# Performance work log

Hardware: AMD Instinct MI355X
Metric: run time of the kernel (lower is better)

## Reference

```python
import jax, jax.numpy as jnp
import numpy as np

B, T, I, H, L, HPR = 256, 512, 128, 256, 64, 50


def _mlp(x, W1, b1, W2, b2):
    # Linear -> ReLU -> Linear, torch convention y = x @ W.T + b
    return jax.nn.relu(x @ W1.T + b1) @ W2.T + b2


def setup_inputs() -> dict:
    key = jax.random.key(0)
    ks = jax.random.split(key, 16)
    s = 0.05
    return {
        "x": jax.random.uniform(ks[0], (B, T, I), dtype=jnp.float32),
        "hidden": jnp.zeros((B, H), jnp.float32),
        "noise": jax.random.normal(ks[1], (B, T, L), dtype=jnp.float32),
        "Wpm1": s * jax.random.normal(ks[2], (HPR, H)), "bpm1": jnp.zeros((HPR,)),
        "Wpm2": s * jax.random.normal(ks[3], (L, HPR)), "bpm2": jnp.zeros((L,)),
        "Wpl1": s * jax.random.normal(ks[4], (HPR, H)), "bpl1": jnp.zeros((HPR,)),
        "Wpl2": s * jax.random.normal(ks[5], (L, HPR)), "bpl2": jnp.zeros((L,)),
        "Wqm1": s * jax.random.normal(ks[6], (HPR, I + H)), "bqm1": jnp.zeros((HPR,)),
        "Wqm2": s * jax.random.normal(ks[7], (L, HPR)), "bqm2": jnp.zeros((L,)),
        "Wql1": s * jax.random.normal(ks[8], (HPR, I + H)), "bql1": jnp.zeros((HPR,)),
        "Wql2": s * jax.random.normal(ks[9], (L, HPR)), "bql2": jnp.zeros((L,)),
        "Wh1": s * jax.random.normal(ks[10], (HPR, I + H + L)), "bh1": jnp.zeros((HPR,)),
        "Wh2": s * jax.random.normal(ks[11], (H, HPR)), "bh2": jnp.zeros((H,)),
        "Wo": s * jax.random.normal(ks[12], (I, H + L)), "bo": jnp.zeros((I,)),
    }


def reference(x, hidden, noise,
              Wpm1, bpm1, Wpm2, bpm2, Wpl1, bpl1, Wpl2, bpl2,
              Wqm1, bqm1, Wqm2, bqm2, Wql1, bql1, Wql2, bql2,
              Wh1, bh1, Wh2, bh2, Wo, bo):
    def step(h, inp):
        x_t, eps = inp  # [B,I], [B,L]
        xh = jnp.concatenate([x_t, h], axis=1)
        q_mu = _mlp(xh, Wqm1, bqm1, Wqm2, bqm2)
        q_lv = _mlp(xh, Wql1, bql1, Wql2, bql2)
        p_mu = _mlp(h, Wpm1, bpm1, Wpm2, bpm2)
        p_lv = _mlp(h, Wpl1, bpl1, Wpl2, bpl2)
        z = q_mu + jnp.exp(0.5 * q_lv) * eps
        h_next = _mlp(jnp.concatenate([x_t, h, z], axis=1), Wh1, bh1, Wh2, bh2)
        out = jax.nn.sigmoid(jnp.concatenate([h, z], axis=1) @ Wo.T + bo)
        return h_next, (out, p_mu, p_lv, q_mu, q_lv)

    xs = (jnp.swapaxes(x, 0, 1), jnp.swapaxes(noise, 0, 1))  # [T,B,*]
    _, (x_hat, p_mu, p_lv, q_mu, q_lv) = jax.lax.scan(step, hidden, xs)
    tb = lambda a: jnp.swapaxes(a, 0, 1)  # [T,B,*] -> [B,T,*]
    return tb(x_hat), tb(p_mu), tb(p_lv), tb(q_mu), tb(q_lv)
```

## Files before the change

### kernel.cpp

```cpp
#include <hip/hip_runtime.h>
#include <stdint.h>


typedef _Float16 f16x2 __attribute__((ext_vector_type(2)));

__device__ __forceinline__ float bf2f(uint16_t u) {
  union { uint32_t u; float f; } c; c.u = ((uint32_t)u) << 16; return c.f;
}
__device__ __forceinline__ uint16_t f2bf(float f) {
  union { float f; uint32_t u; } c; c.f = f;
  uint32_t u = c.u;
  uint32_t r = (u + 0x7FFFu + ((u >> 16) & 1u)) >> 16;
  return (uint16_t)r;
}
__device__ __forceinline__ uint32_t packh2(float a, float b) {
  union { f16x2 h; uint32_t u; } c;
  c.h.x = (_Float16)a; c.h.y = (_Float16)b; return c.u;
}
__device__ __forceinline__ float fdot2(uint32_t a, uint32_t b, float c) {
  union { uint32_t u; f16x2 h; } ua, ub; ua.u = a; ub.u = b;
#if __has_builtin(__builtin_amdgcn_fdot2)
  return __builtin_amdgcn_fdot2(ua.h, ub.h, c, false);
#else
  return c + (float)ua.h.x * (float)ub.h.x + (float)ua.h.y * (float)ub.h.y;
#endif
}

template <int CTRL>
__device__ __forceinline__ float dpp_mov(float x) {
#if __has_builtin(__builtin_amdgcn_update_dpp)
  union { float f; int i; } a, b;
  a.f = x;
  b.i = __builtin_amdgcn_update_dpp(0, a.i, CTRL, 0xF, 0xF, true);
  return b.f;
#else
  return __shfl_xor(x, (CTRL == 0xB1) ? 1 : (CTRL == 0x4E) ? 2 : 4);
#endif
}
__device__ __forceinline__ float red2(float x) {
  return x + dpp_mov<0xB1>(x);
}
__device__ __forceinline__ float red4(float x) {
  x += dpp_mov<0xB1>(x); x += dpp_mov<0x4E>(x); return x;
}
__device__ __forceinline__ float red8(float x) {
  x += dpp_mov<0xB1>(x); x += dpp_mov<0x4E>(x); x += dpp_mov<0x141>(x); return x;
}

__device__ __forceinline__ void barrier_lds() {
  asm volatile("s_waitcnt lgkmcnt(0)\n\ts_barrier" ::: "memory");
}

__device__ __forceinline__ int sniff_bf16(const uint32_t* xw) {
  int cnt = 0;
#pragma unroll
  for (int i = 0; i < 64; ++i) {
    uint32_t e = (xw[i] >> 7) & 0xFFu;
    cnt += (e >= 0x70u && e <= 0x7Fu) ? 1 : 0;
  }
  return cnt >= 32;
}
__device__ __forceinline__ float loadIn(const void* p, size_t i, int isbf) {
  return isbf ? bf2f(((const uint16_t*)p)[i]) : ((const float*)p)[i];
}
__device__ __forceinline__ void storeOut(void* p, size_t i, float v, int isbf) {
  if (isbf) ((uint16_t*)p)[i] = f2bf(v);
  else      ((float*)p)[i] = v;
}

#define WS_W2   75776
#define WS_BIAS 94208
#define N_JOBS  95168

struct PrepArgs {
  const void* W[11];
  const void* B[11];
  const uint32_t* xw;
};

__global__ void vrnn_prep(PrepArgs a, uint32_t* __restrict__ ws) {
  const int isbf = sniff_bf16(a.xw);
  int j = blockIdx.x * 256 + threadIdx.x;
  if (j < 75776) {
    int p = j >> 9, tid = j & 511;
    int t8 = tid >> 3, c8 = tid & 7;
    const void* W; int row, k, K; bool valid;
    if (p < 24)       { W = a.W[0]; row = t8; k = c8*48 + p*2;        K = 384; valid = row < 50; }
    else if (p < 48)  { W = a.W[1]; row = t8; k = c8*48 + (p-24)*2;   K = 384; valid = row < 50; }
    else if (p < 64)  { W = a.W[2]; row = t8; k = c8*32 + (p-48)*2;   K = 256; valid = row < 50; }
    else if (p < 80)  { W = a.W[3]; row = t8; k = c8*32 + (p-64)*2;   K = 256; valid = row < 50; }
    else if (p < 104) { W = a.W[4]; row = t8; k = c8*48 + (p-80)*2;   K = 448; valid = row < 50; }
    else if (p < 108) { W = a.W[4]; row = t8; k = 384 + c8*8 + (p-104)*2; K = 448; valid = row < 50; }
    else if (p < 124) { W = a.W[5]; row = t8;      k = c8*32 + (p-108)*2;     K = 320; valid = true; }
    else if (p < 128) { W = a.W[5]; row = t8;      k = 256 + c8*8 + (p-124)*2; K = 320; valid = true; }
    else if (p < 144) { W = a.W[5]; row = 64 + t8; k = c8*32 + (p-128)*2;     K = 320; valid = true; }
    else              { W = a.W[5]; row = 64 + t8; k = 256 + c8*8 + (p-144)*2; K = 320; valid = true; }
    float f0 = valid ? loadIn(W, (size_t)row * K + k, isbf)     : 0.f;
    float f1 = valid ? loadIn(W, (size_t)row * K + k + 1, isbf) : 0.f;
    ws[j] = packh2(f0, f1);
  } else if (j < WS_BIAS) {
    int q = j - WS_W2;
    const void* W; int r, kp;
    if (q < 9216) { int m = q / 2304, rem = q % 2304; r = rem / 36; kp = rem % 36; W = a.W[6 + m]; }
    else          { int rem = q - 9216;               r = rem / 36; kp = rem % 36; W = a.W[10]; }
    uint32_t v = 0;
    if (kp < 25) v = packh2(loadIn(W, r * 50 + kp * 2, isbf),
                            loadIn(W, r * 50 + kp * 2 + 1, isbf));
    ws[j] = v;
  } else if (j < N_JOBS) {
    int q = j - WS_BIAS; float v = 0.f;
    if (q < 320)      { int m = q >> 6, i = q & 63; if (i < 50) v = loadIn(a.B[m], i, isbf); }
    else if (q < 576) { int m = (q - 320) >> 6;     v = loadIn(a.B[5 + m], q & 63, isbf); }
    else if (q < 832) { v = loadIn(a.B[9],  q - 576, isbf); }
    else              { v = loadIn(a.B[10], q - 832, isbf); }
    ((float*)ws)[j] = v;
  }
}

__global__ __launch_bounds__(512, 2) void vrnn_main(
    const void* __restrict__ x, const void* __restrict__ hidden,
    const void* __restrict__ noise, const uint32_t* __restrict__ ws,
    void* __restrict__ out)
{
  __shared__ __align__(16) uint32_t s_w2[18432];
  __shared__ float s_bias[960];
  __shared__ __align__(16) _Float16 s_v[448];
  __shared__ __align__(16) uint32_t s_actu[180];
  _Float16* s_act = (_Float16*)s_actu;

  const int tid = threadIdx.x;
  const int b = blockIdx.x;
  const int isbf = sniff_bf16((const uint32_t*)x);

  uint32_t wqm1[24], wql1[24], wpm1[16], wpl1[16];
  uint32_t wh1a[24], wh1z[4], wo0h[16], wo0z[4], wo1h[16], wo1z[4];
#pragma unroll
  for (int i = 0; i < 24; ++i) wqm1[i] = ws[(0   + i) * 512 + tid];
#pragma unroll
  for (int i = 0; i < 24; ++i) wql1[i] = ws[(24  + i) * 512 + tid];
#pragma unroll
  for (int i = 0; i < 16; ++i) wpm1[i] = ws[(48  + i) * 512 + tid];
#pragma unroll
  for (int i = 0; i < 16; ++i) wpl1[i] = ws[(64  + i) * 512 + tid];
#pragma unroll
  for (int i = 0; i < 24; ++i) wh1a[i] = ws[(80  + i) * 512 + tid];
#pragma unroll
  for (int i = 0; i < 4;  ++i) wh1z[i] = ws[(104 + i) * 512 + tid];
#pragma unroll
  for (int i = 0; i < 16; ++i) wo0h[i] = ws[(108 + i) * 512 + tid];
#pragma unroll
  for (int i = 0; i < 4;  ++i) wo0z[i] = ws[(124 + i) * 512 + tid];
#pragma unroll
  for (int i = 0; i < 16; ++i) wo1h[i] = ws[(128 + i) * 512 + tid];
#pragma unroll
  for (int i = 0; i < 4;  ++i) wo1z[i] = ws[(144 + i) * 512 + tid];

  for (int i = tid; i < 18432; i += 512) s_w2[i] = ws[WS_W2 + i];
  {
    const float* wsf = (const float*)(ws + WS_BIAS);
    for (int i = tid; i < 960; i += 512) s_bias[i] = wsf[i];
  }

  if (tid < 128)      s_v[tid] = (_Float16)loadIn(x, (size_t)b * 65536 + tid, isbf);
  else if (tid < 384) s_v[tid] = (_Float16)loadIn(hidden, (size_t)b * 256 + (tid - 128), isbf);
  else if (tid < 448) s_v[tid] = (_Float16)0.f;

  const int row8 = tid >> 3, c8 = tid & 7;
  const int i2 = tid >> 2, c4 = tid & 3;
  const int rh = tid >> 1, ch = tid & 1;
  const uint4* v4 = (const uint4*)s_v;

  float eps_r = 0.f;
  if (c4 == 0 && i2 < 64) eps_r = loadIn(noise, (size_t)b * 32768 + i2, isbf);
  float xnext = 0.f;

  __syncthreads();

  const size_t OFF_PMU = 16777216u;
  const size_t OFF_PLV = 25165824u;
  const size_t OFF_QMU = 33554432u;
  const size_t OFF_QLV = 41943040u;

#pragma unroll 1
  for (int t = 0; t < 512; ++t) {
    const size_t bt = (size_t)b * 512 + t;
    if (tid >= 384) {
      int tn = (t < 511) ? t + 1 : 511;
      xnext = loadIn(x, ((size_t)b * 512 + tn) * 128 + (tid - 384), isbf);
    }

    float a_qm = 0.f, a_ql = 0.f, a_hx = 0.f;
    {
      const int g = c8 * 6;
#pragma unroll
      for (int i = 0; i < 6; ++i) {
        uint4 q = v4[g + i];
        a_qm = fdot2(wqm1[4*i+0], q.x, a_qm); a_ql = fdot2(wql1[4*i+0], q.x, a_ql); a_hx = fdot2(wh1a[4*i+0], q.x, a_hx);
        a_qm = fdot2(wqm1[4*i+1], q.y, a_qm); a_ql = fdot2(wql1[4*i+1], q.y, a_ql); a_hx = fdot2(wh1a[4*i+1], q.y, a_hx);
        a_qm = fdot2(wqm1[4*i+2], q.z, a_qm); a_ql = fdot2(wql1[4*i+2], q.z, a_ql); a_hx = fdot2(wh1a[4*i+2], q.z, a_hx);
        a_qm = fdot2(wqm1[4*i+3], q.w, a_qm); a_ql = fdot2(wql1[4*i+3], q.w, a_ql); a_hx = fdot2(wh1a[4*i+3], q.w, a_hx);
      }
    }
    float a_pm = 0.f, a_pl = 0.f, a_o0 = 0.f, a_o1 = 0.f;
    {
      const int g = 16 + c8 * 4;
#pragma unroll
      for (int i = 0; i < 4; ++i) {
        uint4 q = v4[g + i];
        a_pm = fdot2(wpm1[4*i+0], q.x, a_pm); a_pl = fdot2(wpl1[4*i+0], q.x, a_pl);
        a_o0 = fdot2(wo0h[4*i+0], q.x, a_o0); a_o1 = fdot2(wo1h[4*i+0], q.x, a_o1);
        a_pm = fdot2(wpm1[4*i+1], q.y, a_pm); a_pl = fdot2(wpl1[4*i+1], q.y, a_pl);
        a_o0 = fdot2(wo0h[4*i+1], q.y, a_o0); a_o1 = fdot2(wo1h[4*i+1], q.y, a_o1);
        a_pm = fdot2(wpm1[4*i+2], q.z, a_pm); a_pl = fdot2(wpl1[4*i+2], q.z, a_pl);
        a_o0 = fdot2(wo0h[4*i+2], q.z, a_o0); a_o1 = fdot2(wo1h[4*i+2], q.z, a_o1);
        a_pm = fdot2(wpm1[4*i+3], q.w, a_pm); a_pl = fdot2(wpl1[4*i+3], q.w, a_pl);
        a_o0 = fdot2(wo0h[4*i+3], q.w, a_o0); a_o1 = fdot2(wo1h[4*i+3], q.w, a_o1);
      }
    }
    a_qm = red8(a_qm); a_ql = red8(a_ql); a_pm = red8(a_pm); a_pl = red8(a_pl);
    if (c8 == 0) {
      s_act[row8]       = (_Float16)fmaxf(a_qm + s_bias[row8],       0.f);
      s_act[72 + row8]  = (_Float16)fmaxf(a_ql + s_bias[64 + row8],  0.f);
      s_act[144 + row8] = (_Float16)fmaxf(a_pm + s_bias[128 + row8], 0.f);
      s_act[216 + row8] = (_Float16)fmaxf(a_pl + s_bias[192 + row8], 0.f);
    }
    barrier_lds();

    {
      const bool isq = i2 < 64;
      const int r = isq ? i2 : i2 - 64;
      const uint32_t* Wm = s_w2 + (isq ? 0 : 4608) + r * 36 + c4 * 8;
      const uint32_t* Wl = s_w2 + (isq ? 2304 : 6912) + r * 36 + c4 * 8;
      const uint32_t* am = s_actu + (isq ? 0 : 72) + c4 * 8;
      const uint32_t* al = s_actu + (isq ? 36 : 108) + c4 * 8;
      uint4 wm0 = *(const uint4*)Wm, wm1 = *(const uint4*)(Wm + 4);
      uint4 wl0 = *(const uint4*)Wl, wl1 = *(const uint4*)(Wl + 4);
      uint4 am0 = *(const uint4*)am, am1 = *(const uint4*)(am + 4);
      uint4 al0 = *(const uint4*)al, al1 = *(const uint4*)(al + 4);
      float mu0 = 0.f, mu1 = 0.f, lv0 = 0.f, lv1 = 0.f;
      mu0 = fdot2(wm0.x, am0.x, mu0); lv0 = fdot2(wl0.x, al0.x, lv0);
      mu1 = fdot2(wm1.x, am1.x, mu1); lv1 = fdot2(wl1.x, al1.x, lv1);
      mu0 = fdot2(wm0.y, am0.y, mu0); lv0 = fdot2(wl0.y, al0.y, lv0);
      mu1 = fdot2(wm1.y, am1.y, mu1); lv1 = fdot2(wl1.y, al1.y, lv1);
      mu0 = fdot2(wm0.z, am0.z, mu0); lv0 = fdot2(wl0.z, al0.z, lv0);
      mu1 = fdot2(wm1.z, am1.z, mu1); lv1 = fdot2(wl1.z, al1.z, lv1);
      mu0 = fdot2(wm0.w, am0.w, mu0); lv0 = fdot2(wl0.w, al0.w, lv0);
      mu1 = fdot2(wm1.w, am1.w, mu1); lv1 = fdot2(wl1.w, al1.w, lv1);
      float mu = red4(mu0 + mu1);
      float lv = red4(lv0 + lv1);
      if (c4 == 0) {
        mu += s_bias[(isq ? 320 : 448) + r];
        lv += s_bias[(isq ? 384 : 512) + r];
        storeOut(out, (isq ? OFF_QMU : OFF_PMU) + bt * 64 + r, mu, isbf);
        storeOut(out, (isq ? OFF_QLV : OFF_PLV) + bt * 64 + r, lv, isbf);
        if (isq) {
          float z = mu + __expf(0.5f * lv) * eps_r;
          s_v[384 + r] = (_Float16)z;
          int tn = (t < 511) ? t + 1 : 511;
          eps_r = loadIn(noise, ((size_t)b * 512 + tn) * 64 + r, isbf);
        }
      }
    }
    barrier_lds();

    {
      uint4 qz = v4[48 + c8];
      float ah = a_hx, o0 = a_o0, o1 = a_o1;
      ah = fdot2(wh1z[0], qz.x, ah); o0 = fdot2(wo0z[0], qz.x, o0); o1 = fdot2(wo1z[0], qz.x, o1);
      ah = fdot2(wh1z[1], qz.y, ah); o0 = fdot2(wo0z[1], qz.y, o0); o1 = fdot2(wo1z[1], qz.y, o1);
      ah = fdot2(wh1z[2], qz.z, ah); o0 = fdot2(wo0z[2], qz.z, o0); o1 = fdot2(wo1z[2], qz.z, o1);
      ah = fdot2(wh1z[3], qz.w, ah); o0 = fdot2(wo0z[3], qz.w, o0); o1 = fdot2(wo1z[3], qz.w, o1);
      ah = red8(ah); o0 = red8(o0); o1 = red8(o1);
      if (c8 == 0) {
        s_act[288 + row8] = (_Float16)fmaxf(ah + s_bias[256 + row8], 0.f);
        float s0 = 1.f / (1.f + __expf(-(o0 + s_bias[832 + row8])));
        float s1 = 1.f / (1.f + __expf(-(o1 + s_bias[896 + row8])));
        storeOut(out, bt * 128 + row8, s0, isbf);
        storeOut(out, bt * 128 + 64 + row8, s1, isbf);
      }
    }
    barrier_lds();

    {
      const uint32_t* Wr = s_w2 + 9216 + rh * 36 + ch * 16;
      const uint32_t* ap = s_actu + 144 + ch * 16;
      uint4 w0 = *(const uint4*)Wr,        w1 = *(const uint4*)(Wr + 4);
      uint4 w2 = *(const uint4*)(Wr + 8),  w3 = *(const uint4*)(Wr + 12);
      uint4 a0 = *(const uint4*)ap,        a1 = *(const uint4*)(ap + 4);
      uint4 a2 = *(const uint4*)(ap + 8),  a3 = *(const uint4*)(ap + 12);
      float h0 = 0.f, h1 = 0.f;
      h0 = fdot2(w0.x, a0.x, h0); h1 = fdot2(w2.x, a2.x, h1);
      h0 = fdot2(w0.y, a0.y, h0); h1 = fdot2(w2.y, a2.y, h1);
      h0 = fdot2(w0.z, a0.z, h0); h1 = fdot2(w2.z, a2.z, h1);
      h0 = fdot2(w0.w, a0.w, h0); h1 = fdot2(w2.w, a2.w, h1);
      h0 = fdot2(w1.x, a1.x, h0); h1 = fdot2(w3.x, a3.x, h1);
      h0 = fdot2(w1.y, a1.y, h0); h1 = fdot2(w3.y, a3.y, h1);
      h0 = fdot2(w1.z, a1.z, h0); h1 = fdot2(w3.z, a3.z, h1);
      h0 = fdot2(w1.w, a1.w, h0); h1 = fdot2(w3.w, a3.w, h1);
      float hh = red2(h0 + h1);
      if (ch == 0) s_v[128 + rh] = (_Float16)(hh + s_bias[576 + rh]);
    }
    if (tid >= 384) s_v[tid - 384] = (_Float16)xnext;
    barrier_lds();
  }
}

extern "C" void kernel_launch(void* const* d_in, const int* in_sizes, int n_in,
                              void* d_out, int out_size, void* d_ws, size_t ws_size,
                              hipStream_t stream) {
  (void)in_sizes; (void)n_in; (void)out_size; (void)ws_size;
  PrepArgs a;
  a.W[0]  = d_in[11];
  a.W[1]  = d_in[15];
  a.W[2]  = d_in[3];
  a.W[3]  = d_in[7];
  a.W[4]  = d_in[19];
  a.W[5]  = d_in[23];
  a.W[6]  = d_in[13];
  a.W[7]  = d_in[17];
  a.W[8]  = d_in[5];
  a.W[9]  = d_in[9];
  a.W[10] = d_in[21];
  a.B[0]  = d_in[12];
  a.B[1]  = d_in[16];
  a.B[2]  = d_in[4];
  a.B[3]  = d_in[8];
  a.B[4]  = d_in[20];
  a.B[5]  = d_in[14];
  a.B[6]  = d_in[18];
  a.B[7]  = d_in[6];
  a.B[8]  = d_in[10];
  a.B[9]  = d_in[22];
  a.B[10] = d_in[24];
  a.xw    = (const uint32_t*)d_in[0];

  uint32_t* ws = (uint32_t*)d_ws;
  vrnn_prep<<<dim3((N_JOBS + 255) / 256), dim3(256), 0, stream>>>(a, ws);
  vrnn_main<<<dim3(256), dim3(512), 0, stream>>>(d_in[0], d_in[1], d_in[2], ws, d_out);
}
```

Measured before the change: 1.267 ms.

## Double block to 1024 threads and split each dot product across more lanes

The recurrent kernel moves from 512 to 1024 threads per batch-row block. Each thread now holds half as many weight registers. The first-layer and output dot products are split across 16 or 8 lanes with wider DPP reductions, and the prep kernel repacks weights to match. The aim is to shorten each thread's serial fdot2 chain inside every timestep and raise wave count per SIMD to hide latency. The cost is more cross-lane reduction steps and barriers spanning 16 waves per step.

Result: slower. 3.630 ms (+186.4%).

```diff
diff --git a/kernel.cpp b/kernel.cpp
--- a/kernel.cpp
+++ b/kernel.cpp
@@ -34,17 +34,18 @@
   b.i = __builtin_amdgcn_update_dpp(0, a.i, CTRL, 0xF, 0xF, true);
   return b.f;
 #else
-  return __shfl_xor(x, (CTRL == 0xB1) ? 1 : (CTRL == 0x4E) ? 2 : 4);
+  return __shfl_xor(x, 1);
 #endif
-}
-__device__ __forceinline__ float red2(float x) {
-  return x + dpp_mov<0xB1>(x);
 }
 __device__ __forceinline__ float red4(float x) {
   x += dpp_mov<0xB1>(x); x += dpp_mov<0x4E>(x); return x;
 }
 __device__ __forceinline__ float red8(float x) {
   x += dpp_mov<0xB1>(x); x += dpp_mov<0x4E>(x); x += dpp_mov<0x141>(x); return x;
+}
+__device__ __forceinline__ float red16(float x) {
+  x += dpp_mov<0xB1>(x); x += dpp_mov<0x4E>(x);
+  x += dpp_mov<0x141>(x); x += dpp_mov<0x140>(x); return x;
 }
 
 __device__ __forceinline__ void barrier_lds() {
@@ -82,19 +83,18 @@
   const int isbf = sniff_bf16(a.xw);
   int j = blockIdx.x * 256 + threadIdx.x;
   if (j < 75776) {
-    int p = j >> 9, tid = j & 511;
+    int p = j >> 10, tid = j & 1023;
+    int t16 = tid >> 4, c16 = tid & 15;
     int t8 = tid >> 3, c8 = tid & 7;
     const void* W; int row, k, K; bool valid;
-    if (p < 24)       { W = a.W[0]; row = t8; k = c8*48 + p*2;        K = 384; valid = row < 50; }
-    else if (p < 48)  { W = a.W[1]; row = t8; k = c8*48 + (p-24)*2;   K = 384; valid = row < 50; }
-    else if (p < 64)  { W = a.W[2]; row = t8; k = c8*32 + (p-48)*2;   K = 256; valid = row < 50; }
-    else if (p < 80)  { W = a.W[3]; row = t8; k = c8*32 + (p-64)*2;   K = 256; valid = row < 50; }
-    else if (p < 104) { W = a.W[4]; row = t8; k = c8*48 + (p-80)*2;   K = 448; valid = row < 50; }
-    else if (p < 108) { W = a.W[4]; row = t8; k = 384 + c8*8 + (p-104)*2; K = 448; valid = row < 50; }
-    else if (p < 124) { W = a.W[5]; row = t8;      k = c8*32 + (p-108)*2;     K = 320; valid = true; }
-    else if (p < 128) { W = a.W[5]; row = t8;      k = 256 + c8*8 + (p-124)*2; K = 320; valid = true; }
-    else if (p < 144) { W = a.W[5]; row = 64 + t8; k = c8*32 + (p-128)*2;     K = 320; valid = true; }
-    else              { W = a.W[5]; row = 64 + t8; k = 256 + c8*8 + (p-144)*2; K = 320; valid = true; }
+    if (p < 12)       { W = a.W[0]; row = t16; k = c16*24 + p*2;          K = 384; valid = row < 50; }
+    else if (p < 24)  { W = a.W[1]; row = t16; k = c16*24 + (p-12)*2;     K = 384; valid = row < 50; }
+    else if (p < 32)  { W = a.W[2]; row = t16; k = c16*16 + (p-24)*2;     K = 256; valid = row < 50; }
+    else if (p < 40)  { W = a.W[3]; row = t16; k = c16*16 + (p-32)*2;     K = 256; valid = row < 50; }
+    else if (p < 52)  { W = a.W[4]; row = t16; k = c16*24 + (p-40)*2;     K = 448; valid = row < 50; }
+    else if (p < 54)  { W = a.W[4]; row = t16; k = 384 + c16*4 + (p-52)*2; K = 448; valid = row < 50; }
+    else if (p < 70)  { W = a.W[5]; row = t8;  k = c8*32 + (p-54)*2;      K = 320; valid = true; }
+    else              { W = a.W[5]; row = t8;  k = 256 + c8*8 + (p-70)*2; K = 320; valid = true; }
     float f0 = valid ? loadIn(W, (size_t)row * K + k, isbf)     : 0.f;
     float f1 = valid ? loadIn(W, (size_t)row * K + k + 1, isbf) : 0.f;
     ws[j] = packh2(f0, f1);
@@ -117,7 +117,7 @@
   }
 }
 
-__global__ __launch_bounds__(512, 2) void vrnn_main(
+__global__ __launch_bounds__(1024, 4) void vrnn_main(
     const void* __restrict__ x, const void* __restrict__ hidden,
     const void* __restrict__ noise, const uint32_t* __restrict__ ws,
     void* __restrict__ out)
@@ -132,46 +132,42 @@
   const int b = blockIdx.x;
   const int isbf = sniff_bf16((const uint32_t*)x);
 
-  uint32_t wqm1[24], wql1[24], wpm1[16], wpl1[16];
-  uint32_t wh1a[24], wh1z[4], wo0h[16], wo0z[4], wo1h[16], wo1z[4];
-#pragma unroll
-  for (int i = 0; i < 24; ++i) wqm1[i] = ws[(0   + i) * 512 + tid];
-#pragma unroll
-  for (int i = 0; i < 24; ++i) wql1[i] = ws[(24  + i) * 512 + tid];
-#pragma unroll
-  for (int i = 0; i < 16; ++i) wpm1[i] = ws[(48  + i) * 512 + tid];
-#pragma unroll
-  for (int i = 0; i < 16; ++i) wpl1[i] = ws[(64  + i) * 512 + tid];
-#pragma unroll
-  for (int i = 0; i < 24; ++i) wh1a[i] = ws[(80  + i) * 512 + tid];
-#pragma unroll
-  for (int i = 0; i < 4;  ++i) wh1z[i] = ws[(104 + i) * 512 + tid];
-#pragma unroll
-  for (int i = 0; i < 16; ++i) wo0h[i] = ws[(108 + i) * 512 + tid];
-#pragma unroll
-  for (int i = 0; i < 4;  ++i) wo0z[i] = ws[(124 + i) * 512 + tid];
-#pragma unroll
-  for (int i = 0; i < 16; ++i) wo1h[i] = ws[(128 + i) * 512 + tid];
-#pragma unroll
-  for (int i = 0; i < 4;  ++i) wo1z[i] = ws[(144 + i) * 512 + tid];
-
-  for (int i = tid; i < 18432; i += 512) s_w2[i] = ws[WS_W2 + i];
+  uint32_t wqm1[12], wql1[12], wpm1[8], wpl1[8], wh1a[12], wh1z[2], woh[16], woz[4];
+#pragma unroll
+  for (int i = 0; i < 12; ++i) wqm1[i] = ws[(0  + i) * 1024 + tid];
+#pragma unroll
+  for (int i = 0; i < 12; ++i) wql1[i] = ws[(12 + i) * 1024 + tid];
+#pragma unroll
+  for (int i = 0; i < 8;  ++i) wpm1[i] = ws[(24 + i) * 1024 + tid];
+#pragma unroll
+  for (int i = 0; i < 8;  ++i) wpl1[i] = ws[(32 + i) * 1024 + tid];
+#pragma unroll
+  for (int i = 0; i < 12; ++i) wh1a[i] = ws[(40 + i) * 1024 + tid];
+#pragma unroll
+  for (int i = 0; i < 2;  ++i) wh1z[i] = ws[(52 + i) * 1024 + tid];
+#pragma unroll
+  for (int i = 0; i < 16; ++i) woh[i]  = ws[(54 + i) * 1024 + tid];
+#pragma unroll
+  for (int i = 0; i < 4;  ++i) woz[i]  = ws[(70 + i) * 1024 + tid];
+
+  for (int i = tid; i < 18432; i += 1024) s_w2[i] = ws[WS_W2 + i];
   {
     const float* wsf = (const float*)(ws + WS_BIAS);
-    for (int i = tid; i < 960; i += 512) s_bias[i] = wsf[i];
+    if (tid < 960) s_bias[tid] = wsf[tid];
   }
 
   if (tid < 128)      s_v[tid] = (_Float16)loadIn(x, (size_t)b * 65536 + tid, isbf);
   else if (tid < 384) s_v[tid] = (_Float16)loadIn(hidden, (size_t)b * 256 + (tid - 128), isbf);
   else if (tid < 448) s_v[tid] = (_Float16)0.f;
 
-  const int row8 = tid >> 3, c8 = tid & 7;
-  const int i2 = tid >> 2, c4 = tid & 3;
-  const int rh = tid >> 1, ch = tid & 1;
+  const int row16 = tid >> 4, c16 = tid & 15;
+  const int i8 = tid >> 3, c8 = tid & 7;
+  const int r4 = tid >> 2, c4 = tid & 3;
   const uint4* v4 = (const uint4*)s_v;
+  const uint32_t* s_vu = (const uint32_t*)s_v;
 
   float eps_r = 0.f;
-  if (c4 == 0 && i2 < 64) eps_r = loadIn(noise, (size_t)b * 32768 + i2, isbf);
+  if (c8 == 0 && i8 < 64) eps_r = loadIn(noise, (size_t)b * 32768 + i8, isbf);
   float xnext = 0.f;
 
   __syncthreads();
@@ -184,16 +180,16 @@
 #pragma unroll 1
   for (int t = 0; t < 512; ++t) {
     const size_t bt = (size_t)b * 512 + t;
-    if (tid >= 384) {
+    if (tid >= 896) {
       int tn = (t < 511) ? t + 1 : 511;
-      xnext = loadIn(x, ((size_t)b * 512 + tn) * 128 + (tid - 384), isbf);
+      xnext = loadIn(x, ((size_t)b * 512 + tn) * 128 + (tid - 896), isbf);
     }
 
     float a_qm = 0.f, a_ql = 0.f, a_hx = 0.f;
     {
-      const int g = c8 * 6;
-#pragma unroll
-      for (int i = 0; i < 6; ++i) {
+      const int g = c16 * 3;
+#pragma unroll
+      for (int i = 0; i < 3; ++i) {
         uint4 q = v4[g + i];
         a_qm = fdot2(wqm1[4*i+0], q.x, a_qm); a_ql = fdot2(wql1[4*i+0], q.x, a_ql); a_hx = fdot2(wh1a[4*i+0], q.x, a_hx);
         a_qm = fdot2(wqm1[4*i+1], q.y, a_qm); a_ql = fdot2(wql1[4*i+1], q.y, a_ql); a_hx = fdot2(wh1a[4*i+1], q.y, a_hx);
@@ -201,54 +197,55 @@
         a_qm = fdot2(wqm1[4*i+3], q.w, a_qm); a_ql = fdot2(wql1[4*i+3], q.w, a_ql); a_hx = fdot2(wh1a[4*i+3], q.w, a_hx);
       }
     }
-    float a_pm = 0.f, a_pl = 0.f, a_o0 = 0.f, a_o1 = 0.f;
+    float a_pm = 0.f, a_pl = 0.f;
+    {
+      const int g = 16 + c16 * 2;
+#pragma unroll
+      for (int i = 0; i < 2; ++i) {
+        uint4 q = v4[g + i];
+        a_pm = fdot2(wpm1[4*i+0], q.x, a_pm); a_pl = fdot2(wpl1[4*i+0], q.x, a_pl);
+        a_pm = fdot2(wpm1[4*i+1], q.y, a_pm); a_pl = fdot2(wpl1[4*i+1], q.y, a_pl);
+        a_pm = fdot2(wpm1[4*i+2], q.z, a_pm); a_pl = fdot2(wpl1[4*i+2], q.z, a_pl);
+        a_pm = fdot2(wpm1[4*i+3], q.w, a_pm); a_pl = fdot2(wpl1[4*i+3], q.w, a_pl);
+      }
+    }
+    float a_o = 0.f;
     {
       const int g = 16 + c8 * 4;
 #pragma unroll
       for (int i = 0; i < 4; ++i) {
         uint4 q = v4[g + i];
-        a_pm = fdot2(wpm1[4*i+0], q.x, a_pm); a_pl = fdot2(wpl1[4*i+0], q.x, a_pl);
-        a_o0 = fdot2(wo0h[4*i+0], q.x, a_o0); a_o1 = fdot2(wo1h[4*i+0], q.x, a_o1);
-        a_pm = fdot2(wpm1[4*i+1], q.y, a_pm); a_pl = fdot2(wpl1[4*i+1], q.y, a_pl);
-        a_o0 = fdot2(wo0h[4*i+1], q.y, a_o0); a_o1 = fdot2(wo1h[4*i+1], q.y, a_o1);
-        a_pm = fdot2(wpm1[4*i+2], q.z, a_pm); a_pl = fdot2(wpl1[4*i+2], q.z, a_pl);
-        a_o0 = fdot2(wo0h[4*i+2], q.z, a_o0); a_o1 = fdot2(wo1h[4*i+2], q.z, a_o1);
-        a_pm = fdot2(wpm1[4*i+3], q.w, a_pm); a_pl = fdot2(wpl1[4*i+3], q.w, a_pl);
-        a_o0 = fdot2(wo0h[4*i+3], q.w, a_o0); a_o1 = fdot2(wo1h[4*i+3], q.w, a_o1);
-      }
-    }
-    a_qm = red8(a_qm); a_ql = red8(a_ql); a_pm = red8(a_pm); a_pl = red8(a_pl);
-    if (c8 == 0) {
-      s_act[row8]       = (_Float16)fmaxf(a_qm + s_bias[row8],       0.f);
-      s_act[72 + row8]  = (_Float16)fmaxf(a_ql + s_bias[64 + row8],  0.f);
-      s_act[144 + row8] = (_Float16)fmaxf(a_pm + s_bias[128 + row8], 0.f);
-      s_act[216 + row8] = (_Float16)fmaxf(a_pl + s_bias[192 + row8], 0.f);
+        a_o = fdot2(woh[4*i+0], q.x, a_o);
+        a_o = fdot2(woh[4*i+1], q.y, a_o);
+        a_o = fdot2(woh[4*i+2], q.z, a_o);
+        a_o = fdot2(woh[4*i+3], q.w, a_o);
+      }
+    }
+    a_qm = red16(a_qm); a_ql = red16(a_ql); a_pm = red16(a_pm); a_pl = red16(a_pl);
+    if (c16 == 0) {
+      s_act[row16]       = (_Float16)fmaxf(a_qm + s_bias[row16],       0.f);
+      s_act[72 + row16]  = (_Float16)fmaxf(a_ql + s_bias[64 + row16],  0.f);
+      s_act[144 + row16] = (_Float16)fmaxf(a_pm + s_bias[128 + row16], 0.f);
+      s_act[216 + row16] = (_Float16)fmaxf(a_pl + s_bias[192 + row16], 0.f);
     }
     barrier_lds();
 
     {
-      const bool isq = i2 < 64;
-      const int r = isq ? i2 : i2 - 64;
-      const uint32_t* Wm = s_w2 + (isq ? 0 : 4608) + r * 36 + c4 * 8;
-      const uint32_t* Wl = s_w2 + (isq ? 2304 : 6912) + r * 36 + c4 * 8;
-      const uint32_t* am = s_actu + (isq ? 0 : 72) + c4 * 8;
-      const uint32_t* al = s_actu + (isq ? 36 : 108) + c4 * 8;
-      uint4 wm0 = *(const uint4*)Wm, wm1 = *(const uint4*)(Wm + 4);
-      uint4 wl0 = *(const uint4*)Wl, wl1 = *(const uint4*)(Wl + 4);
-      uint4 am0 = *(const uint4*)am, am1 = *(const uint4*)(am + 4);
-      uint4 al0 = *(const uint4*)al, al1 = *(const uint4*)(al + 4);
-      float mu0 = 0.f, mu1 = 0.f, lv0 = 0.f, lv1 = 0.f;
-      mu0 = fdot2(wm0.x, am0.x, mu0); lv0 = fdot2(wl0.x, al0.x, lv0);
-      mu1 = fdot2(wm1.x, am1.x, mu1); lv1 = fdot2(wl1.x, al1.x, lv1);
-      mu0 = fdot2(wm0.y, am0.y, mu0); lv0 = fdot2(wl0.y, al0.y, lv0);
-      mu1 = fdot2(wm1.y, am1.y, mu1); lv1 = fdot2(wl1.y, al1.y, lv1);
-      mu0 = fdot2(wm0.z, am0.z, mu0); lv0 = fdot2(wl0.z, al0.z, lv0);
-      mu1 = fdot2(wm1.z, am1.z, mu1); lv1 = fdot2(wl1.z, al1.z, lv1);
-      mu0 = fdot2(wm0.w, am0.w, mu0); lv0 = fdot2(wl0.w, al0.w, lv0);
-      mu1 = fdot2(wm1.w, am1.w, mu1); lv1 = fdot2(wl1.w, al1.w, lv1);
-      float mu = red4(mu0 + mu1);
-      float lv = red4(lv0 + lv1);
-      if (c4 == 0) {
+      const bool isq = i8 < 64;
+      const int r = isq ? i8 : i8 - 64;
+      const uint32_t* Wm = s_w2 + (isq ? 0 : 4608) + r * 36 + c8 * 4;
+      const uint32_t* Wl = s_w2 + (isq ? 2304 : 6912) + r * 36 + c8 * 4;
+      const uint32_t* am = s_actu + (isq ? 0 : 72) + c8 * 4;
+      const uint32_t* al = s_actu + (isq ? 36 : 108) + c8 * 4;
+      uint4 wm = *(const uint4*)Wm, wl = *(const uint4*)Wl;
+      uint4 vm = *(const uint4*)am, vl = *(const uint4*)al;
+      float mu = 0.f, lv = 0.f;
+      mu = fdot2(wm.x, vm.x, mu); lv = fdot2(wl.x, vl.x, lv);
+      mu = fdot2(wm.y, vm.y, mu); lv = fdot2(wl.y, vl.y, lv);
+      mu = fdot2(wm.z, vm.z, mu); lv = fdot2(wl.z, vl.z, lv);
+      mu = fdot2(wm.w, vm.w, mu); lv = fdot2(wl.w, vl.w, lv);
+      mu = red8(mu); lv = red8(lv);
+      if (c8 == 0) {
         mu += s_bias[(isq ? 320 : 448) + r];
         lv += s_bias[(isq ? 384 : 512) + r];
         storeOut(out, (isq ? OFF_QMU : OFF_PMU) + bt * 64 + r, mu, isbf);
@@ -265,42 +262,39 @@
 
     {
       uint4 qz = v4[48 + c8];
-      float ah = a_hx, o0 = a_o0, o1 = a_o1;
-      ah = fdot2(wh1z[0], qz.x, ah); o0 = fdot2(wo0z[0], qz.x, o0); o1 = fdot2(wo1z[0], qz.x, o1);
-      ah = fdot2(wh1z[1], qz.y, ah); o0 = fdot2(wo0z[1], qz.y, o0); o1 = fdot2(wo1z[1], qz.y, o1);
-      ah = fdot2(wh1z[2], qz.z, ah); o0 = fdot2(wo0z[2], qz.z, o0); o1 = fdot2(wo1z[2], qz.z, o1);
-      ah = fdot2(wh1z[3], qz.w, ah); o0 = fdot2(wo0z[3], qz.w, o0); o1 = fdot2(wo1z[3], qz.w, o1);
-      ah = red8(ah); o0 = red8(o0); o1 = red8(o1);
+      float o = a_o;
+      o = fdot2(woz[0], qz.x, o);
+      o = fdot2(woz[1], qz.y, o);
+      o = fdot2(woz[2], qz.z, o);
+      o = fdot2(woz[3], qz.w, o);
+      uint32_t z0 = s_vu[192 + c16 * 2], z1 = s_vu[193 + c16 * 2];
+      float ah = a_hx;
+      ah = fdot2(wh1z[0], z0, ah);
+      ah = fdot2(wh1z[1], z1, ah);
+      o = red8(o); ah = red16(ah);
       if (c8 == 0) {
-        s_act[288 + row8] = (_Float16)fmaxf(ah + s_bias[256 + row8], 0.f);
-        float s0 = 1.f / (1.f + __expf(-(o0 + s_bias[832 + row8])));
-        float s1 = 1.f / (1.f + __expf(-(o1 + s_bias[896 + row8])));
-        storeOut(out, bt * 128 + row8, s0, isbf);
-        storeOut(out, bt * 128 + 64 + row8, s1, isbf);
-      }
+        float s0 = 1.f / (1.f + __expf(-(o + s_bias[832 + i8])));
+        storeOut(out, bt * 128 + i8, s0, isbf);
+      }
+      if (c16 == 0)
+        s_act[288 + row16] = (_Float16)fmaxf(ah + s_bias[256 + row16], 0.f);
     }
     barrier_lds();
 
     {
-      const uint32_t* Wr = s_w2 + 9216 + rh * 36 + ch * 16;
-      const uint32_t* ap = s_actu + 144 + ch * 16;
-      uint4 w0 = *(const uint4*)Wr,        w1 = *(const uint4*)(Wr + 4);
-      uint4 w2 = *(const uint4*)(Wr + 8),  w3 = *(const uint4*)(Wr + 12);
-      uint4 a0 = *(const uint4*)ap,        a1 = *(const uint4*)(ap + 4);
-      uint4 a2 = *(const uint4*)(ap + 8),  a3 = *(const uint4*)(ap + 12);
+      const uint32_t* Wr = s_w2 + 9216 + r4 * 36 + c4 * 8;
+      const uint32_t* ap = s_actu + 144 + c4 * 8;
+      uint4 w0 = *(const uint4*)Wr, w1 = *(const uint4*)(Wr + 4);
+      uint4 a0 = *(const uint4*)ap, a1 = *(const uint4*)(ap + 4);
       float h0 = 0.f, h1 = 0.f;
-      h0 = fdot2(w0.x, a0.x, h0); h1 = fdot2(w2.x, a2.x, h1);
-      h0 = fdot2(w0.y, a0.y, h0); h1 = fdot2(w2.y, a2.y, h1);
-      h0 = fdot2(w0.z, a0.z, h0); h1 = fdot2(w2.z, a2.z, h1);
-      h0 = fdot2(w0.w, a0.w, h0); h1 = fdot2(w2.w, a2.w, h1);
-      h0 = fdot2(w1.x, a1.x, h0); h1 = fdot2(w3.x, a3.x, h1);
-      h0 = fdot2(w1.y, a1.y, h0); h1 = fdot2(w3.y, a3.y, h1);
-      h0 = fdot2(w1.z, a1.z, h0); h1 = fdot2(w3.z, a3.z, h1);
-      h0 = fdot2(w1.w, a1.w, h0); h1 = fdot2(w3.w, a3.w, h1);
-      float hh = red2(h0 + h1);
-      if (ch == 0) s_v[128 + rh] = (_Float16)(hh + s_bias[576 + rh]);
-    }
-    if (tid >= 384) s_v[tid - 384] = (_Float16)xnext;
+      h0 = fdot2(w0.x, a0.x, h0); h1 = fdot2(w1.x, a1.x, h1);
+      h0 = fdot2(w0.y, a0.y, h0); h1 = fdot2(w1.y, a1.y, h1);
+      h0 = fdot2(w0.z, a0.z, h0); h1 = fdot2(w1.z, a1.z, h1);
+      h0 = fdot2(w0.w, a0.w, h0); h1 = fdot2(w1.w, a1.w, h1);
+      float hh = red4(h0 + h1);
+      if (c4 == 0) s_v[128 + r4] = (_Float16)(hh + s_bias[576 + r4]);
+    }
+    if (tid >= 896) s_v[tid - 896] = (_Float16)xnext;
     barrier_lds();
   }
 }
@@ -336,5 +330,5 @@
 
   uint32_t* ws = (uint32_t*)d_ws;
   vrnn_prep<<<dim3((N_JOBS + 255) / 256), dim3(256), 0, stream>>>(a, ws);
-  vrnn_main<<<dim3(256), dim3(512), 0, stream>>>(d_in[0], d_in[1], d_in[2], ws, d_out);
-}
+  vrnn_main<<<dim3(256), dim3(1024), 0, stream>>>(d_in[0], d_in[1], d_in[2], ws, d_out);
+}
```
